# Optimization experiments

Hardware: AMD Instinct MI355X
Metric: run time of the kernel (lower is better)

## Reference

```python
import jax, jax.numpy as jnp
import numpy as np

IN_FEATURES = 4096
OUT_FEATURES = 16384
TOKENS = 32


def setup_inputs() -> dict:
    key = jax.random.key(0)
    k1, k2, k3, k4 = jax.random.split(key, 4)
    x = jax.random.normal(k1, (TOKENS, IN_FEATURES), dtype=jnp.float16)
    # int8-valued weights in [-127, 127]
    weight_int8 = jax.random.randint(k2, (OUT_FEATURES, IN_FEATURES), -127, 128, dtype=jnp.int32)
    # per-output-channel scale, positive (amax/127 in the original)
    scale = (jax.random.uniform(k3, (OUT_FEATURES,), dtype=jnp.float32) * 0.02 + 1e-4).astype(jnp.float16)
    bias = jax.random.normal(k4, (OUT_FEATURES,), dtype=jnp.float16)
    return {"x": x, "weight_int8": weight_int8, "scale": scale, "bias": bias}


def reference(x, weight_int8, scale, bias):
    # Dequantize int8 weights to compute dtype with per-row scale, then linear.
    w = weight_int8.astype(jnp.float16) * scale[:, None]          # [out, in] fp16
    return jnp.dot(x, w.T) + bias                                  # [tokens, out]
```

## Files before the change

kernel.cpp:

```cpp
#include <hip/hip_runtime.h>
#include <hip/hip_bf16.h>


typedef __attribute__((ext_vector_type(4))) int    i32x4;
typedef __attribute__((ext_vector_type(4))) float  f32x4;
typedef __attribute__((ext_vector_type(8))) short  s16x8;
typedef __attribute__((ext_vector_type(8))) __bf16 bf16x8;

constexpr int K = 4096;
constexpr int N = 16384;

__device__ inline unsigned short f2bf_rne(float f) {
    unsigned u = __builtin_bit_cast(unsigned, f);
    u += 0x7FFF + ((u >> 16) & 1);
    return (unsigned short)(u >> 16);
}

__device__ inline bf16x8 cvtW(i32x4 lo, i32x4 hi) {
    s16x8 r;
#pragma unroll
    for (int i = 0; i < 4; ++i) {
        r[i]     = (short)(__builtin_bit_cast(unsigned, (float)lo[i]) >> 16);
        r[i + 4] = (short)(__builtin_bit_cast(unsigned, (float)hi[i]) >> 16);
    }
    return __builtin_bit_cast(s16x8, r), __builtin_bit_cast(bf16x8, r);
}

__device__ inline bf16x8 cvtX(f32x4 lo, f32x4 hi) {
    s16x8 r;
#pragma unroll
    for (int i = 0; i < 4; ++i) {
        r[i]     = (short)f2bf_rne(lo[i]);
        r[i + 4] = (short)f2bf_rne(hi[i]);
    }
    return __builtin_bit_cast(bf16x8, r);
}

__global__ __launch_bounds__(256, 1) void w8linear_kernel(
    const float* __restrict__ x,
    const int* __restrict__ w,
    const float* __restrict__ scale,
    const float* __restrict__ bias,
    float* __restrict__ out)
{
    const int lane = threadIdx.x & 63;
    const int wave = threadIdx.x >> 6;
    const int n16  = lane & 15;
    const int quad = lane >> 4;

    const int c = blockIdx.x * 64 + wave * 16 + n16;

    const int*   __restrict__ wrow  = w + (size_t)c * K;
    const float* __restrict__ xrow0 = x + (size_t)n16 * K;
    const float* __restrict__ xrow1 = x + (size_t)(n16 + 16) * K;

    f32x4 acc0 = {0.f, 0.f, 0.f, 0.f};
    f32x4 acc1 = {0.f, 0.f, 0.f, 0.f};

    i32x4 bA[8], bB[8];
    f32x4 aA[16], aB[16];

    auto load_chunk = [&](int k0, i32x4* bb, f32x4* ax) {
#pragma unroll
        for (int s = 0; s < 4; ++s) {
            const int ks = k0 + 32 * s + quad * 8;
            bb[2 * s]     = *reinterpret_cast<const i32x4*>(wrow + ks);
            bb[2 * s + 1] = *reinterpret_cast<const i32x4*>(wrow + ks + 4);
            ax[4 * s]     = *reinterpret_cast<const f32x4*>(xrow0 + ks);
            ax[4 * s + 1] = *reinterpret_cast<const f32x4*>(xrow0 + ks + 4);
            ax[4 * s + 2] = *reinterpret_cast<const f32x4*>(xrow1 + ks);
            ax[4 * s + 3] = *reinterpret_cast<const f32x4*>(xrow1 + ks + 4);
        }
    };
    auto compute_chunk = [&](const i32x4* bb, const f32x4* ax) {
#pragma unroll
        for (int s = 0; s < 4; ++s) {
            bf16x8 bf = cvtW(bb[2 * s], bb[2 * s + 1]);
            bf16x8 a0 = cvtX(ax[4 * s], ax[4 * s + 1]);
            bf16x8 a1 = cvtX(ax[4 * s + 2], ax[4 * s + 3]);
            acc0 = __builtin_amdgcn_mfma_f32_16x16x32_bf16(a0, bf, acc0, 0, 0, 0);
            acc1 = __builtin_amdgcn_mfma_f32_16x16x32_bf16(a1, bf, acc1, 0, 0, 0);
        }
    };

    load_chunk(0, bA, aA);
#pragma unroll 1
    for (int k0 = 0; k0 < K; k0 += 256) {
        load_chunk(k0 + 128, bB, aB);
        compute_chunk(bA, aA);
        if (k0 + 256 < K) load_chunk(k0 + 256, bA, aA);
        compute_chunk(bB, aB);
    }

    const float sc = scale[c];
    const float bi = bias[c];
#pragma unroll
    for (int v = 0; v < 4; ++v) {
        const int row = quad * 4 + v;
        out[(size_t)row * N + c]        = acc0[v] * sc + bi;
        out[(size_t)(row + 16) * N + c] = acc1[v] * sc + bi;
    }
}

extern "C" void kernel_launch(void* const* d_in, const int* in_sizes, int n_in,
                              void* d_out, int out_size, void* d_ws, size_t ws_size,
                              hipStream_t stream) {
    const float* x     = (const float*)d_in[0];
    const int*   w     = (const int*)d_in[1];
    const float* scale = (const float*)d_in[2];
    const float* bias  = (const float*)d_in[3];
    float* out = (float*)d_out;

    dim3 grid(N / 64);
    dim3 block(256);
    w8linear_kernel<<<grid, block, 0, stream>>>(x, w, scale, bias, out);
}
```

Before: 387.1 us.

## Split-K the int8 GEMM with bf16 pre-converted activations and reduction kernel

```diff
diff --git a/kernel.cpp b/kernel.cpp
--- a/kernel.cpp
+++ b/kernel.cpp
@@ -9,6 +9,11 @@
 
 constexpr int K = 4096;
 constexpr int N = 16384;
+constexpr int T = 32;
+constexpr int KSPLIT = 4;
+constexpr int KPW = K / KSPLIT;
+constexpr size_t XB_OFF = 0;
+constexpr size_t PART_OFF = 262144;
 
 __device__ inline unsigned short f2bf_rne(float f) {
     unsigned u = __builtin_bit_cast(unsigned, f);
@@ -23,83 +28,107 @@
         r[i]     = (short)(__builtin_bit_cast(unsigned, (float)lo[i]) >> 16);
         r[i + 4] = (short)(__builtin_bit_cast(unsigned, (float)hi[i]) >> 16);
     }
-    return __builtin_bit_cast(s16x8, r), __builtin_bit_cast(bf16x8, r);
-}
-
-__device__ inline bf16x8 cvtX(f32x4 lo, f32x4 hi) {
-    s16x8 r;
-#pragma unroll
-    for (int i = 0; i < 4; ++i) {
-        r[i]     = (short)f2bf_rne(lo[i]);
-        r[i + 4] = (short)f2bf_rne(hi[i]);
-    }
     return __builtin_bit_cast(bf16x8, r);
 }
 
-__global__ __launch_bounds__(256, 1) void w8linear_kernel(
-    const float* __restrict__ x,
+__global__ __launch_bounds__(256) void xcvt_kernel(const float* __restrict__ x,
+                                                   unsigned short* __restrict__ xb) {
+    const int i = (blockIdx.x * 256 + threadIdx.x) * 8;
+    f32x4 lo = *reinterpret_cast<const f32x4*>(x + i);
+    f32x4 hi = *reinterpret_cast<const f32x4*>(x + i + 4);
+    s16x8 r;
+#pragma unroll
+    for (int j = 0; j < 4; ++j) {
+        r[j]     = (short)f2bf_rne(lo[j]);
+        r[j + 4] = (short)f2bf_rne(hi[j]);
+    }
+    *reinterpret_cast<s16x8*>(xb + i) = r;
+}
+
+__global__ __launch_bounds__(256, 4) void w8gemm_kernel(
+    const __bf16* __restrict__ xb,
     const int* __restrict__ w,
-    const float* __restrict__ scale,
-    const float* __restrict__ bias,
-    float* __restrict__ out)
+    float* __restrict__ partial)
 {
     const int lane = threadIdx.x & 63;
     const int wave = threadIdx.x >> 6;
     const int n16  = lane & 15;
     const int quad = lane >> 4;
 
-    const int c = blockIdx.x * 64 + wave * 16 + n16;
+    const int g  = blockIdx.x & 255;
+    const int ks = blockIdx.x >> 8;
 
-    const int*   __restrict__ wrow  = w + (size_t)c * K;
-    const float* __restrict__ xrow0 = x + (size_t)n16 * K;
-    const float* __restrict__ xrow1 = x + (size_t)(n16 + 16) * K;
+    const int c = g * 64 + wave * 16 + n16;
+    const int k0 = ks * KPW;
+
+    const int*   __restrict__ wrow = w + (size_t)c * K + k0;
+    const __bf16* __restrict__ xr0 = xb + (size_t)n16 * K + k0;
+    const __bf16* __restrict__ xr1 = xb + (size_t)(n16 + 16) * K + k0;
 
     f32x4 acc0 = {0.f, 0.f, 0.f, 0.f};
     f32x4 acc1 = {0.f, 0.f, 0.f, 0.f};
 
-    i32x4 bA[8], bB[8];
-    f32x4 aA[16], aB[16];
+    i32x4 bA[4], bB[4];
+    bf16x8 aA[4], aB[4];
 
-    auto load_chunk = [&](int k0, i32x4* bb, f32x4* ax) {
-#pragma unroll
-        for (int s = 0; s < 4; ++s) {
-            const int ks = k0 + 32 * s + quad * 8;
-            bb[2 * s]     = *reinterpret_cast<const i32x4*>(wrow + ks);
-            bb[2 * s + 1] = *reinterpret_cast<const i32x4*>(wrow + ks + 4);
-            ax[4 * s]     = *reinterpret_cast<const f32x4*>(xrow0 + ks);
-            ax[4 * s + 1] = *reinterpret_cast<const f32x4*>(xrow0 + ks + 4);
-            ax[4 * s + 2] = *reinterpret_cast<const f32x4*>(xrow1 + ks);
-            ax[4 * s + 3] = *reinterpret_cast<const f32x4*>(xrow1 + ks + 4);
-        }
+    auto load_chunk = [&](int kc, i32x4* bb, bf16x8* aa) {
+        const int e0 = kc + quad * 8;
+        const int e1 = e0 + 32;
+        bb[0] = *reinterpret_cast<const i32x4*>(wrow + e0);
+        bb[1] = *reinterpret_cast<const i32x4*>(wrow + e0 + 4);
+        bb[2] = *reinterpret_cast<const i32x4*>(wrow + e1);
+        bb[3] = *reinterpret_cast<const i32x4*>(wrow + e1 + 4);
+        aa[0] = *reinterpret_cast<const bf16x8*>(xr0 + e0);
+        aa[1] = *reinterpret_cast<const bf16x8*>(xr1 + e0);
+        aa[2] = *reinterpret_cast<const bf16x8*>(xr0 + e1);
+        aa[3] = *reinterpret_cast<const bf16x8*>(xr1 + e1);
     };
-    auto compute_chunk = [&](const i32x4* bb, const f32x4* ax) {
-#pragma unroll
-        for (int s = 0; s < 4; ++s) {
-            bf16x8 bf = cvtW(bb[2 * s], bb[2 * s + 1]);
-            bf16x8 a0 = cvtX(ax[4 * s], ax[4 * s + 1]);
-            bf16x8 a1 = cvtX(ax[4 * s + 2], ax[4 * s + 3]);
-            acc0 = __builtin_amdgcn_mfma_f32_16x16x32_bf16(a0, bf, acc0, 0, 0, 0);
-            acc1 = __builtin_amdgcn_mfma_f32_16x16x32_bf16(a1, bf, acc1, 0, 0, 0);
-        }
+    auto compute_chunk = [&](const i32x4* bb, const bf16x8* aa) {
+        bf16x8 bf0 = cvtW(bb[0], bb[1]);
+        acc0 = __builtin_amdgcn_mfma_f32_16x16x32_bf16(aa[0], bf0, acc0, 0, 0, 0);
+        acc1 = __builtin_amdgcn_mfma_f32_16x16x32_bf16(aa[1], bf0, acc1, 0, 0, 0);
+        bf16x8 bf1 = cvtW(bb[2], bb[3]);
+        acc0 = __builtin_amdgcn_mfma_f32_16x16x32_bf16(aa[2], bf1, acc0, 0, 0, 0);
+        acc1 = __builtin_amdgcn_mfma_f32_16x16x32_bf16(aa[3], bf1, acc1, 0, 0, 0);
     };
 
     load_chunk(0, bA, aA);
 #pragma unroll 1
-    for (int k0 = 0; k0 < K; k0 += 256) {
-        load_chunk(k0 + 128, bB, aB);
+    for (int kc = 0; kc < KPW; kc += 128) {
+        load_chunk(kc + 64, bB, aB);
         compute_chunk(bA, aA);
-        if (k0 + 256 < K) load_chunk(k0 + 256, bA, aA);
+        if (kc + 128 < KPW) load_chunk(kc + 128, bA, aA);
         compute_chunk(bB, aB);
     }
 
-    const float sc = scale[c];
-    const float bi = bias[c];
+    float* __restrict__ p = partial + (size_t)ks * T * N;
 #pragma unroll
     for (int v = 0; v < 4; ++v) {
         const int row = quad * 4 + v;
-        out[(size_t)row * N + c]        = acc0[v] * sc + bi;
-        out[(size_t)(row + 16) * N + c] = acc1[v] * sc + bi;
+        p[(size_t)row * N + c]        = acc0[v];
+        p[(size_t)(row + 16) * N + c] = acc1[v];
     }
+}
+
+__global__ __launch_bounds__(256) void reduce_kernel(
+    const float* __restrict__ partial,
+    const float* __restrict__ scale,
+    const float* __restrict__ bias,
+    float* __restrict__ out)
+{
+    const int i = (blockIdx.x * 256 + threadIdx.x) * 4;
+    const int c = i & (N - 1);
+    f32x4 s = *reinterpret_cast<const f32x4*>(partial + i);
+#pragma unroll
+    for (int ks = 1; ks < KSPLIT; ++ks) {
+        f32x4 pv = *reinterpret_cast<const f32x4*>(partial + (size_t)ks * T * N + i);
+        s[0] += pv[0]; s[1] += pv[1]; s[2] += pv[2]; s[3] += pv[3];
+    }
+    f32x4 sc = *reinterpret_cast<const f32x4*>(scale + c);
+    f32x4 bi = *reinterpret_cast<const f32x4*>(bias + c);
+    f32x4 r = {s[0] * sc[0] + bi[0], s[1] * sc[1] + bi[1],
+               s[2] * sc[2] + bi[2], s[3] * sc[3] + bi[3]};
+    *reinterpret_cast<f32x4*>(out + i) = r;
 }
 
 extern "C" void kernel_launch(void* const* d_in, const int* in_sizes, int n_in,
@@ -111,7 +140,12 @@
     const float* bias  = (const float*)d_in[3];
     float* out = (float*)d_out;
 
-    dim3 grid(N / 64);
-    dim3 block(256);
-    w8linear_kernel<<<grid, block, 0, stream>>>(x, w, scale, bias, out);
+    unsigned short* xb = (unsigned short*)((char*)d_ws + XB_OFF);
+    float* part        = (float*)((char*)d_ws + PART_OFF);
+
+    xcvt_kernel<<<dim3(64), dim3(256), 0, stream>>>(x, xb);
+    w8gemm_kernel<<<dim3(256 * KSPLIT), dim3(256), 0, stream>>>(
+        (const __bf16*)xb, w, part);
+    reduce_kernel<<<dim3((T * N / 4) / 256), dim3(256), 0, stream>>>(
+        part, scale, bias, out);
 }
```

After: 389.1 us. Within noise of the previous version (+0.5%).
